# Kernel tuning notes

Hardware: AMD Instinct MI355X
Metric: run time of the kernel (lower is better)

## Reference

```python
import jax, jax.numpy as jnp
import numpy as np

B, T, H, F, E = 512, 32, 768, 3072, 3  # E = num_route_experts = num_experts - 1 (top-1 beam)


def setup_inputs() -> dict:
    key = jax.random.key(0)
    ks = jax.random.split(key, 4)
    s = 0.02
    return {
        "x": jax.random.normal(ks[0], (B, T, H), jnp.float32),
        "Wg": jax.random.normal(ks[1], (E, H), jnp.float32) * s,
        "W1": jax.random.normal(ks[2], (E, H, F), jnp.float32) * s,
        "b1": jnp.zeros((E, F), jnp.float32),
        "W2": jax.random.normal(ks[3], (E, F, H), jnp.float32) * s,
        "b2": jnp.zeros((E, H), jnp.float32),
    }


def reference(x, Wg, W1, b1, W2, b2):
    # forward_gate: mean-pool over tokens (attention_mask is all-ones), linear gate, softmax
    scores = jax.nn.softmax(jnp.mean(x, axis=1) @ Wg.T, axis=-1)  # [B, E]
    # beam_search, first layer with num_route_beam=1: plain top-1 expert selection
    _, idx = jax.lax.top_k(scores, 1)
    sel = idx[:, 0]  # [B] int32, selected expert per sample
    # forward_expert_ffn: densely run EVERY route expert (gelu MLP) on the full batch
    h = jax.nn.gelu(jnp.einsum('bth,ehf->betf', x, W1) + b1[None, :, None, :], approximate=False)  # [B,E,T,F]
    y = jnp.einsum('betf,efh->beth', h, W2) + b2[None, :, None, :]  # [B,E,T,H]
    # weight_type == 'ffn_prob': one-hot mask times gate prob, then sum over experts
    w = scores * jax.nn.one_hot(sel, E, dtype=scores.dtype)  # [B, E]
    out = jnp.einsum('beth,be->bth', y, w)  # [B, T, H]
    return out
```

## Files before the change

kernel.cpp:

```cpp
#include <hip/hip_runtime.h>
#include <hip/hip_bf16.h>
#include <cstdint>
#include <cstddef>

namespace {

constexpr int kB = 512, kT = 32, kH = 768, kF = 3072, kE = 3;
constexpr int kMaxTiles = 131;
constexpr int kMaxChunk = 131;
constexpr int kHbufTile  = 128 * kF;
constexpr int kXconvB = kT * kH;

typedef __attribute__((ext_vector_type(8))) short short8;
typedef __attribute__((ext_vector_type(4))) float f32x4;

__device__ __forceinline__ void gld_lds16(const void* g, void* l) {
  __builtin_amdgcn_global_load_lds(
      (const __attribute__((address_space(1))) void*)g,
      (__attribute__((address_space(3))) void*)l, 16, 0, 0);
}

__device__ __forceinline__ float bf2f(__hip_bfloat16 v) { return __bfloat162float(v); }
__device__ __forceinline__ float bfu(unsigned short u) {
  return __uint_as_float(((unsigned)u) << 16);
}
__device__ __forceinline__ unsigned short f2bfb(float f) {
  __hip_bfloat16 h = __float2bfloat16(f);
  return *reinterpret_cast<unsigned short*>(&h);
}

__device__ __forceinline__ float gelu_f(float v) {
  float av = fabsf(v);
  float z = av * 0.70710678118654752f;
  float t = __builtin_amdgcn_rcpf(fmaf(0.3275911f, z, 1.0f));
  float p = fmaf(fmaf(fmaf(fmaf(1.061405429f, t, -1.453152027f), t, 1.421413741f),
                      t, -0.284496736f), t, 0.254829592f) * t;
  float er = fmaf(-p, __expf(-z * z), 1.0f);
  return 0.5f * v + 0.5f * av * er;
}

__global__ __launch_bounds__(256)
void k_prep_x(const void* __restrict__ xv, const void* __restrict__ Wgv,
              float* __restrict__ wsel,
              int* __restrict__ cntTk,
              int* __restrict__ lists,
              int* __restrict__ tileExpert, int* __restrict__ tileBatch,
              int* __restrict__ numTiles,
              __hip_bfloat16* __restrict__ xconv) {
  __shared__ __align__(16) unsigned short xs[32][772];
  __shared__ float red[3][256];
  __shared__ int sniffX, sniffG, lastFlag;
  __shared__ int csh[3];
  int b = blockIdx.x, tid = threadIdx.x;
  if (tid == 0) { sniffX = 0; sniffG = 0; }
  __syncthreads();
  {
    const unsigned short* xw = (const unsigned short*)xv;
    const unsigned short* gw = (const unsigned short*)Wgv;
    int lx = 0, lg = 0;
#pragma unroll
    for (int i = 0; i < 16; ++i) lx += (((xw[tid + 256 * i] >> 7) & 0xFF) >= 0xC0);
#pragma unroll
    for (int i = 0; i < 8; ++i) lg += (((gw[tid + 256 * i] >> 7) & 0xFF) >= 0xC0);
    atomicAdd(&sniffX, lx);
    atomicAdd(&sniffG, lg);
  }
  __syncthreads();
  bool fx = (sniffX > 64), fg = (sniffG > 32);

  float a0 = 0.f, a1 = 0.f, a2 = 0.f;
  if (tid < 192) {
    float m0 = 0.f, m1 = 0.f, m2 = 0.f, m3 = 0.f;
    if (fx) {
      const float4* xr = (const float4*)((const float*)xv + (size_t)b * kT * kH) + tid;
#pragma unroll 8
      for (int t = 0; t < kT; ++t) {
        float4 u = xr[t * 192];
        m0 += u.x; m1 += u.y; m2 += u.z; m3 += u.w;
        ushort4 v;
        v.x = f2bfb(u.x); v.y = f2bfb(u.y); v.z = f2bfb(u.z); v.w = f2bfb(u.w);
        *(ushort4*)&xs[t][tid * 4] = v;
      }
    } else {
      const ushort4* xr = (const ushort4*)((const unsigned short*)xv + (size_t)b * kT * kH) + tid;
#pragma unroll 8
      for (int t = 0; t < kT; ++t) {
        ushort4 u = xr[t * 192];
        m0 += bfu(u.x); m1 += bfu(u.y); m2 += bfu(u.z); m3 += bfu(u.w);
        *(ushort4*)&xs[t][tid * 4] = u;
      }
    }
    const float inv = 1.f / kT;
    m0 *= inv; m1 *= inv; m2 *= inv; m3 *= inv;
#pragma unroll
    for (int e = 0; e < kE; ++e) {
      float w0, w1v, w2v, w3;
      int base = e * kH + tid * 4;
      if (fg) {
        float4 u = *(const float4*)((const float*)Wgv + base);
        w0 = u.x; w1v = u.y; w2v = u.z; w3 = u.w;
      } else {
        ushort4 u = *(const ushort4*)((const unsigned short*)Wgv + base);
        w0 = bfu(u.x); w1v = bfu(u.y); w2v = bfu(u.z); w3 = bfu(u.w);
      }
      float d = m0 * w0 + m1 * w1v + m2 * w2v + m3 * w3;
      if (e == 0) a0 = d; else if (e == 1) a1 = d; else a2 = d;
    }
  }
  red[0][tid] = a0; red[1][tid] = a1; red[2][tid] = a2;
  __syncthreads();
  for (int s2 = 128; s2 > 0; s2 >>= 1) {
    if (tid < s2) {
      red[0][tid] += red[0][tid + s2];
      red[1][tid] += red[1][tid + s2];
      red[2][tid] += red[2][tid + s2];
    }
    __syncthreads();
  }
  if (tid == 0) {
    float l0 = red[0][0], l1 = red[1][0], l2 = red[2][0];
    int am = 0; float mx = l0;
    if (l1 > mx) { mx = l1; am = 1; }
    if (l2 > mx) { mx = l2; am = 2; }
    float e0 = expf(l0 - mx), e1 = expf(l1 - mx), e2 = expf(l2 - mx);
    float inv = 1.f / (e0 + e1 + e2);
    float sc = (am == 0 ? e0 : (am == 1 ? e1 : e2)) * inv;
    wsel[b] = sc;
    int pos = atomicAdd(&cntTk[am], 1);
    lists[am * kB + pos] = b;
    __threadfence();
    int tk = atomicAdd(&cntTk[3], 1);
    lastFlag = (tk == kB - 1) ? 1 : 0;
  }

  __syncthreads();
  unsigned short* dst = (unsigned short*)xconv + (size_t)b * kXconvB;
#pragma unroll
  for (int i = 0; i < 12; ++i) {
    int g = i * 256 + tid;
    int t32 = g >> 7, r = g & 127, mm = r >> 2, qp = r & 3;
    int col = t32 * 32 + (qp ^ ((mm >> 1) & 3)) * 8;
    ushort4 lo = *(const ushort4*)&xs[mm][col];
    ushort4 hi = *(const ushort4*)&xs[mm][col + 4];
    short8 v;
    v[0] = lo.x; v[1] = lo.y; v[2] = lo.z; v[3] = lo.w;
    v[4] = hi.x; v[5] = hi.y; v[6] = hi.z; v[7] = hi.w;
    *(short8*)(dst + g * 8) = v;
  }

  if (lastFlag) {
    __threadfence();
    if (tid < 3) csh[tid] = cntTk[tid];
    __syncthreads();
    int c0 = csh[0], c1 = csh[1], c2 = csh[2];
    int t0 = ((c0 + 3) & ~3) >> 2;
    int t1 = ((c1 + 3) & ~3) >> 2;
    int t2 = ((c2 + 3) & ~3) >> 2;
    int total = t0 + t1 + t2;
    if (tid == 0) *numTiles = total;
    for (int t = tid; t < kMaxTiles; t += 256) {
      int e = 0, base = 0, cc = 0;
      bool pad = false;
      if (t < t0) { e = 0; base = t; cc = c0; }
      else if (t < t0 + t1) { e = 1; base = t - t0; cc = c1; }
      else if (t < total) { e = 2; base = t - t0 - t1; cc = c2; }
      else pad = true;
      if (pad) {
        tileExpert[t] = 0;
        for (int s = 0; s < 4; ++s) tileBatch[t * 4 + s] = -1;
      } else {
        tileExpert[t] = e;
        for (int s = 0; s < 4; ++s) {
          int i = base * 4 + s;
          tileBatch[t * 4 + s] = (i < cc) ? lists[e * kB + i] : -1;
        }
      }
    }
  }
}

__global__ __launch_bounds__(256)
void k_transpose6(const void* __restrict__ w1src, const void* __restrict__ w2src,
                  __hip_bfloat16* __restrict__ w1dst, __hip_bfloat16* __restrict__ w2dst) {
  int z = blockIdx.z;
  bool isW1 = (z < 3);
  int e = isW1 ? z : z - 3;
  __shared__ __align__(16) unsigned short t[64][73];
  __shared__ int cnt_s;
  if (threadIdx.x == 0) cnt_s = 0;
  __syncthreads();
  {
    const unsigned short* hw = (const unsigned short*)(isW1 ? w1src : w2src);
    int local = 0;
#pragma unroll
    for (int i = 0; i < 16; ++i)
      local += (((hw[threadIdx.x + 256 * i] >> 7) & 0xFF) >= 0xC0);
    atomicAdd(&cnt_s, local);
  }
  __syncthreads();
  bool f32 = (cnt_s > 64);
  const float* sf = (const float*)(isW1 ? w1src : w2src);
  const unsigned short* sb = (const unsigned short*)(isW1 ? w1src : w2src);
  unsigned short* dst = (unsigned short*)(isW1 ? w1dst : w2dst);
  int K = isW1 ? kH : kF, N = isW1 ? kF : kH;
  int ntx = N / 64;
  int bx = blockIdx.x;
  int n0 = (bx % ntx) * 64, k0 = (bx / ntx) * 64;
  size_t eoff = (size_t)e * K * N;
  int tr = threadIdx.x >> 4;
  int tc4 = (threadIdx.x & 15) * 4;
#pragma unroll
  for (int i = 0; i < 4; ++i) {
    int r = tr + 16 * i;
    size_t idx = eoff + (size_t)(k0 + r) * N + n0 + tc4;
    if (f32) {
      float4 u = *(const float4*)(sf + idx);
      t[r][tc4] = f2bfb(u.x); t[r][tc4 + 1] = f2bfb(u.y);
      t[r][tc4 + 2] = f2bfb(u.z); t[r][tc4 + 3] = f2bfb(u.w);
    } else {
      ushort4 u = *(const ushort4*)(sb + idx);
      t[r][tc4] = u.x; t[r][tc4 + 1] = u.y; t[r][tc4 + 2] = u.z; t[r][tc4 + 3] = u.w;
    }
  }
  __syncthreads();
#pragma unroll
  for (int i = 0; i < 4; ++i) {
    int rn = tr + 16 * i;
    ushort4 v;
    v.x = t[tc4][rn]; v.y = t[tc4 + 1][rn]; v.z = t[tc4 + 2][rn]; v.w = t[tc4 + 3][rn];
    *(ushort4*)(dst + eoff + (size_t)(n0 + rn) * K + k0 + tc4) = v;
  }
}

__global__ __launch_bounds__(256, 2)
void k_ffn1(const __hip_bfloat16* __restrict__ xconv,
            const __hip_bfloat16* __restrict__ w1t,
            const __hip_bfloat16* __restrict__ b1,
            const int* __restrict__ tileExpert,
            const int* __restrict__ tileBatch,
            const int* __restrict__ numTiles,
            int tileOff,
            __hip_bfloat16* __restrict__ hbuf) {
  int j = blockIdx.y;
  int local = j / 3;
  int tile = local + tileOff;
  if (tile >= *numTiles) return;
  int nIdx = 8 * (j % 3) + blockIdx.x;
  int nbase = nIdx * 128;
  int e = tileExpert[tile];
  __shared__ __align__(16) short ldsbuf[16384];
  short* ldsA = ldsbuf;
  short* ldsB = ldsbuf + 8192;
  int tid = threadIdx.x;
  int lane = tid & 63, wid = tid >> 6;
  int wm = wid >> 1, wn = wid & 1;
  int lane16 = lane & 15, qf = lane >> 4;
  int swzl = (lane16 >> 1) & 3;
  int qx = (qf ^ swzl) * 8;

  int slotLo = tid >> 7;
  int b0v = tileBatch[tile * 4];
  int bLo = tileBatch[tile * 4 + slotLo];
  int bHi = tileBatch[tile * 4 + 2 + slotLo];
  if (bLo < 0) bLo = b0v;
  if (bHi < 0) bHi = b0v;
  int mmLo = (tid >> 2) & 31;
  int q = (tid & 3) ^ ((tid >> 3) & 3);
  int qp = q ^ ((mmLo >> 1) & 3);
  int baseOff = (mmLo * 4 + qp) * 8;
  const __hip_bfloat16* pLo = xconv + (size_t)bLo * kXconvB + baseOff;
  const __hip_bfloat16* pHi = xconv + (size_t)bHi * kXconvB + baseOff;

  f32x4 acc[4][4];
#pragma unroll
  for (int r = 0; r < 4; ++r)
#pragma unroll
    for (int c = 0; c < 4; ++c) acc[r][c] = (f32x4)0.f;

  const __hip_bfloat16* w1e = w1t + (size_t)e * kF * kH;
  const __hip_bfloat16* gB[4];
  short* lB[4];
#pragma unroll
  for (int it = 0; it < 4; ++it) {
    int s = it * 256 + tid;
    int m = (s >> 2) & 127, kk = s >> 9;
    int qq = (s & 3) ^ ((s >> 3) & 3);
    gB[it] = w1e + (size_t)(nbase + m) * kH + kk * 32 + qq * 8;
    lB[it] = &ldsB[s * 8];
  }

  for (int k0 = 0; k0 < kH; k0 += 64) {
    int koff = (k0 >> 6) * 2048;
    gld_lds16(pLo + koff,        &ldsA[(0 * 256 + tid) * 8]);
    gld_lds16(pHi + koff,        &ldsA[(1 * 256 + tid) * 8]);
    gld_lds16(pLo + koff + 1024, &ldsA[(2 * 256 + tid) * 8]);
    gld_lds16(pHi + koff + 1024, &ldsA[(3 * 256 + tid) * 8]);
#pragma unroll
    for (int it = 0; it < 4; ++it) gld_lds16(gB[it] + k0, lB[it]);
    __syncthreads();
#pragma unroll
    for (int kk = 0; kk < 2; ++kk) {
      short8 af[4], bfr[4];
#pragma unroll
      for (int r = 0; r < 4; ++r) {
        int mr = wm * 64 + r * 16 + lane16;
        af[r] = *(const short8*)&ldsA[(kk * 512 + mr * 4) * 8 + qx];
      }
#pragma unroll
      for (int c = 0; c < 4; ++c) {
        int mb = wn * 64 + c * 16 + lane16;
        bfr[c] = *(const short8*)&ldsB[(kk * 512 + mb * 4) * 8 + qx];
      }
#pragma unroll
      for (int r = 0; r < 4; ++r)
#pragma unroll
        for (int c = 0; c < 4; ++c)
          acc[r][c] = __builtin_amdgcn_mfma_f32_16x16x32_bf16(af[r], bfr[c], acc[r][c], 0, 0, 0);
    }
    __syncthreads();
  }

  __hip_bfloat16* htile = hbuf + (size_t)local * kHbufTile;
  unsigned short* uls = (unsigned short*)ldsbuf;
  int q4 = qf * 4;
#pragma unroll
  for (int c = 0; c < 4; ++c) {
    int nn = wn * 64 + c * 16 + lane16;
    float bias = bf2f(b1[e * kF + nbase + nn]);
    int lbase = (nn >> 6) * 8192 + ((nn >> 5) & 1) * 4096 + (nn & 7);
    int qn = (nn >> 3) & 3;
#pragma unroll
    for (int r = 0; r < 4; ++r) {
#pragma unroll
      for (int g = 0; g < 4; ++g) {
        int m = wm * 64 + r * 16 + q4 + g;
        float v = acc[r][c][g] + bias;
        uls[lbase + (m * 4 + (qn ^ ((m >> 1) & 3))) * 8] = f2bfb(gelu_f(v));
      }
    }
  }
  __syncthreads();
  unsigned short* dstg = (unsigned short*)htile + (size_t)(nbase >> 6) * 8192;
#pragma unroll
  for (int i = 0; i < 8; ++i) {
    int s = i * 2048 + tid * 8;
    *(short8*)(dstg + s) = *(const short8*)(uls + s);
  }
}

__global__ __launch_bounds__(256, 2)
void k_ffn2(const __hip_bfloat16* __restrict__ hbuf,
            const __hip_bfloat16* __restrict__ w2t,
            const __hip_bfloat16* __restrict__ b2,
            const float* __restrict__ wsel,
            const int* __restrict__ tileExpert,
            const int* __restrict__ tileBatch,
            const int* __restrict__ numTiles,
            int tileOff, int chunk,
            float* __restrict__ out) {
  int j = blockIdx.y;
  int local = blockIdx.x + 8 * (j / 6);
  if (local >= chunk) return;
  int tile = local + tileOff;
  if (tile >= *numTiles) return;
  int nbase = (j % 6) * 128;
  int e = tileExpert[tile];
  int tbraw[4];
  float sc[4];
#pragma unroll
  for (int s = 0; s < 4; ++s) {
    int bb = tileBatch[tile * 4 + s];
    tbraw[s] = bb;
    sc[s] = (bb >= 0) ? wsel[bb] : 0.f;
  }
  __shared__ __align__(16) short ldsA[8192];
  __shared__ __align__(16) short ldsB[8192];
  int tid = threadIdx.x;
  int lane = tid & 63, wid = tid >> 6;
  int wm = wid >> 1, wn = wid & 1;
  int lane16 = lane & 15, qf = lane >> 4;
  int swzl = (lane16 >> 1) & 3;
  int qx = (qf ^ swzl) * 8;

  f32x4 acc[4][4];
#pragma unroll
  for (int r = 0; r < 4; ++r)
#pragma unroll
    for (int c = 0; c < 4; ++c) acc[r][c] = (f32x4)0.f;

  const __hip_bfloat16* w2e = w2t + (size_t)e * kF * kH;
  const __hip_bfloat16* htile = hbuf + (size_t)local * kHbufTile;
  const __hip_bfloat16* gB[4];
  short* lA[4];
  short* lB[4];
  int aoff[4];
#pragma unroll
  for (int it = 0; it < 4; ++it) {
    int s = it * 256 + tid;
    int m = (s >> 2) & 127, kk = s >> 9;
    int qq = (s & 3) ^ ((s >> 3) & 3);
    aoff[it] = s * 8;
    gB[it] = w2e + (size_t)(nbase + m) * kF + kk * 32 + qq * 8;
    lA[it] = &ldsA[s * 8];
    lB[it] = &ldsB[s * 8];
  }

  for (int k0 = 0; k0 < kF; k0 += 64) {
#pragma unroll
    for (int it = 0; it < 4; ++it) gld_lds16(htile + k0 * 128 + aoff[it], lA[it]);
#pragma unroll
    for (int it = 0; it < 4; ++it) gld_lds16(gB[it] + k0, lB[it]);
    __syncthreads();
#pragma unroll
    for (int kk = 0; kk < 2; ++kk) {
      short8 af[4], bfr[4];
#pragma unroll
      for (int r = 0; r < 4; ++r) {
        int mr = wm * 64 + r * 16 + lane16;
        af[r] = *(const short8*)&ldsA[(kk * 512 + mr * 4) * 8 + qx];
      }
#pragma unroll
      for (int c = 0; c < 4; ++c) {
        int mb = wn * 64 + c * 16 + lane16;
        bfr[c] = *(const short8*)&ldsB[(kk * 512 + mb * 4) * 8 + qx];
      }
#pragma unroll
      for (int r = 0; r < 4; ++r)
#pragma unroll
        for (int c = 0; c < 4; ++c)
          acc[r][c] = __builtin_amdgcn_mfma_f32_16x16x32_bf16(af[r], bfr[c], acc[r][c], 0, 0, 0);
    }
    __syncthreads();
  }

  int q4 = qf * 4;
#pragma unroll
  for (int c = 0; c < 4; ++c) {
    int ncol = wn * 64 + c * 16 + lane16;
    float bias = bf2f(b2[e * kH + nbase + ncol]);
#pragma unroll
    for (int r = 0; r < 4; ++r) {
      int s = (wm * 64 + r * 16) >> 5;
      int bb = tbraw[s];
      if (bb < 0) continue;
      float scale = sc[s];
#pragma unroll
      for (int g = 0; g < 4; ++g) {
        int m = wm * 64 + r * 16 + q4 + g;
        float v = (acc[r][c][g] + bias) * scale;
        out[((size_t)(bb * kT + (m & 31))) * kH + nbase + ncol] = v;
      }
    }
  }
}

}

extern "C" void kernel_launch(void* const* d_in, const int* in_sizes, int n_in,
                              void* d_out, int out_size, void* d_ws, size_t ws_size,
                              hipStream_t stream) {
  (void)in_sizes; (void)n_in; (void)out_size;
  float* out = (float*)d_out;

  char* ws = (char*)d_ws;
  size_t off = 0;
  auto alloc = [&](size_t bytes) -> char* {
    char* p = ws + off;
    off = (off + bytes + 255) & ~(size_t)255;
    return p;
  };
  int*   cntTk      = (int*)alloc(16);
  float* wsel       = (float*)alloc(kB * 4);
  int*   lists      = (int*)alloc((size_t)kE * kB * 4);
  int*   tileExpert = (int*)alloc(kMaxTiles * 4);
  int*   tileBatch  = (int*)alloc(kMaxTiles * 4 * 4);
  int*   numTiles   = (int*)alloc(4);
  __hip_bfloat16* w1t   = (__hip_bfloat16*)alloc((size_t)kE * kH * kF * 2);
  __hip_bfloat16* w2t   = (__hip_bfloat16*)alloc((size_t)kE * kH * kF * 2);
  __hip_bfloat16* xconv = (__hip_bfloat16*)alloc((size_t)kB * kXconvB * 2);

  size_t tileBytes = (size_t)kHbufTile * 2;
  size_t avail = (ws_size > off + tileBytes) ? (ws_size - off) : tileBytes;
  int chunk = (int)(avail / tileBytes);
  if (chunk > kMaxChunk) chunk = kMaxChunk;
  if (chunk < 1) chunk = 1;
  __hip_bfloat16* hbuf = (__hip_bfloat16*)alloc((size_t)chunk * tileBytes);

  hipMemsetAsync(cntTk, 0, 16, stream);
  k_prep_x<<<kB, 256, 0, stream>>>(d_in[0], d_in[1], wsel, cntTk, lists,
                                   tileExpert, tileBatch, numTiles, xconv);
  k_transpose6<<<dim3(576, 1, 6), 256, 0, stream>>>(d_in[2], d_in[4], w1t, w2t);
  for (int toff = 0; toff < kMaxTiles; toff += chunk) {
    k_ffn1<<<dim3(8, 3 * chunk), 256, 0, stream>>>(xconv, w1t,
                                                   (const __hip_bfloat16*)d_in[3],
                                                   tileExpert, tileBatch,
                                                   numTiles, toff, hbuf);
    int rows2 = (chunk + 7) / 8;
    k_ffn2<<<dim3(8, 6 * rows2), 256, 0, stream>>>(hbuf, w2t,
                                                   (const __hip_bfloat16*)d_in[5], wsel,
                                                   tileExpert, tileBatch, numTiles,
                                                   toff, chunk, out);
  }
}
```

Baseline: 378.0 us.

## Rewrite FFN1 as 256x256 double-buffered GEMM with fused prep/transpose launch

Merges the x-prep and weight-transpose kernels into one launch, which saves a kernel boundary. FFN1 moves to 512-thread blocks that compute two 128-row tiles against a 256-wide N slab. Operand loads go straight from global memory into LDS and are double-buffered, with explicit waitcnt, barriers and setprio interleaving so loads overlap MFMA work. Tile padding now rounds experts to pairs of tiles so each block handles two tiles of the same expert. The cost is higher register and LDS pressure (128KB dynamic LDS), and some extra padded tiles.

```diff
diff --git a/kernel.cpp b/kernel.cpp
--- a/kernel.cpp
+++ b/kernel.cpp
@@ -6,9 +6,9 @@
 namespace {
 
 constexpr int kB = 512, kT = 32, kH = 768, kF = 3072, kE = 3;
-constexpr int kMaxTiles = 131;
-constexpr int kMaxChunk = 131;
-constexpr int kHbufTile  = 128 * kF;
+constexpr int kMaxTiles = 132;
+constexpr int kMaxChunk = 132;
+constexpr int kHbufTile = 128 * kF;
 constexpr int kXconvB = kT * kH;
 
 typedef __attribute__((ext_vector_type(8))) short short8;
@@ -40,311 +40,375 @@
 }
 
 __global__ __launch_bounds__(256)
-void k_prep_x(const void* __restrict__ xv, const void* __restrict__ Wgv,
-              float* __restrict__ wsel,
-              int* __restrict__ cntTk,
-              int* __restrict__ lists,
-              int* __restrict__ tileExpert, int* __restrict__ tileBatch,
-              int* __restrict__ numTiles,
-              __hip_bfloat16* __restrict__ xconv) {
-  __shared__ __align__(16) unsigned short xs[32][772];
-  __shared__ float red[3][256];
-  __shared__ int sniffX, sniffG, lastFlag;
-  __shared__ int csh[3];
-  int b = blockIdx.x, tid = threadIdx.x;
-  if (tid == 0) { sniffX = 0; sniffG = 0; }
-  __syncthreads();
-  {
-    const unsigned short* xw = (const unsigned short*)xv;
-    const unsigned short* gw = (const unsigned short*)Wgv;
-    int lx = 0, lg = 0;
-#pragma unroll
-    for (int i = 0; i < 16; ++i) lx += (((xw[tid + 256 * i] >> 7) & 0xFF) >= 0xC0);
-#pragma unroll
-    for (int i = 0; i < 8; ++i) lg += (((gw[tid + 256 * i] >> 7) & 0xFF) >= 0xC0);
-    atomicAdd(&sniffX, lx);
-    atomicAdd(&sniffG, lg);
-  }
-  __syncthreads();
-  bool fx = (sniffX > 64), fg = (sniffG > 32);
-
-  float a0 = 0.f, a1 = 0.f, a2 = 0.f;
-  if (tid < 192) {
-    float m0 = 0.f, m1 = 0.f, m2 = 0.f, m3 = 0.f;
-    if (fx) {
-      const float4* xr = (const float4*)((const float*)xv + (size_t)b * kT * kH) + tid;
+void k_prep(const void* __restrict__ xv, const void* __restrict__ Wgv,
+            const void* __restrict__ w1src, const void* __restrict__ w2src,
+            float* __restrict__ wsel, int* __restrict__ cntTk,
+            int* __restrict__ lists, int* __restrict__ tileExpert,
+            int* __restrict__ tileBatch, int* __restrict__ numTiles,
+            __hip_bfloat16* __restrict__ xconv,
+            __hip_bfloat16* __restrict__ w1dst, __hip_bfloat16* __restrict__ w2dst) {
+  __shared__ __align__(16) char smem[52992];
+  __shared__ int ish[6];
+  int tid = threadIdx.x;
+  if (blockIdx.x < (unsigned)kB) {
+    auto xs = (unsigned short (*)[772])smem;
+    float (*red)[256] = (float (*)[256])(smem + 49408);
+    int b = blockIdx.x;
+    if (tid == 0) { ish[0] = 0; ish[1] = 0; }
+    __syncthreads();
+    {
+      const unsigned short* xw = (const unsigned short*)xv;
+      const unsigned short* gw = (const unsigned short*)Wgv;
+      int lx = 0, lg = 0;
+#pragma unroll
+      for (int i = 0; i < 16; ++i) lx += (((xw[tid + 256 * i] >> 7) & 0xFF) >= 0xC0);
+#pragma unroll
+      for (int i = 0; i < 8; ++i) lg += (((gw[tid + 256 * i] >> 7) & 0xFF) >= 0xC0);
+      atomicAdd(&ish[0], lx);
+      atomicAdd(&ish[1], lg);
+    }
+    __syncthreads();
+    bool fx = (ish[0] > 64), fg = (ish[1] > 32);
+    float a0 = 0.f, a1 = 0.f, a2 = 0.f;
+    if (tid < 192) {
+      float m0 = 0.f, m1 = 0.f, m2 = 0.f, m3 = 0.f;
+      if (fx) {
+        const float4* xr = (const float4*)((const float*)xv + (size_t)b * kT * kH) + tid;
 #pragma unroll 8
-      for (int t = 0; t < kT; ++t) {
-        float4 u = xr[t * 192];
-        m0 += u.x; m1 += u.y; m2 += u.z; m3 += u.w;
-        ushort4 v;
-        v.x = f2bfb(u.x); v.y = f2bfb(u.y); v.z = f2bfb(u.z); v.w = f2bfb(u.w);
-        *(ushort4*)&xs[t][tid * 4] = v;
-      }
-    } else {
-      const ushort4* xr = (const ushort4*)((const unsigned short*)xv + (size_t)b * kT * kH) + tid;
+        for (int t = 0; t < kT; ++t) {
+          float4 u = xr[t * 192];
+          m0 += u.x; m1 += u.y; m2 += u.z; m3 += u.w;
+          ushort4 v;
+          v.x = f2bfb(u.x); v.y = f2bfb(u.y); v.z = f2bfb(u.z); v.w = f2bfb(u.w);
+          *(ushort4*)&xs[t][tid * 4] = v;
+        }
+      } else {
+        const ushort4* xr = (const ushort4*)((const unsigned short*)xv + (size_t)b * kT * kH) + tid;
 #pragma unroll 8
-      for (int t = 0; t < kT; ++t) {
-        ushort4 u = xr[t * 192];
-        m0 += bfu(u.x); m1 += bfu(u.y); m2 += bfu(u.z); m3 += bfu(u.w);
-        *(ushort4*)&xs[t][tid * 4] = u;
-      }
-    }
-    const float inv = 1.f / kT;
-    m0 *= inv; m1 *= inv; m2 *= inv; m3 *= inv;
-#pragma unroll
-    for (int e = 0; e < kE; ++e) {
-      float w0, w1v, w2v, w3;
-      int base = e * kH + tid * 4;
-      if (fg) {
-        float4 u = *(const float4*)((const float*)Wgv + base);
-        w0 = u.x; w1v = u.y; w2v = u.z; w3 = u.w;
+        for (int t = 0; t < kT; ++t) {
+          ushort4 u = xr[t * 192];
+          m0 += bfu(u.x); m1 += bfu(u.y); m2 += bfu(u.z); m3 += bfu(u.w);
+          *(ushort4*)&xs[t][tid * 4] = u;
+        }
+      }
+      const float inv = 1.f / kT;
+      m0 *= inv; m1 *= inv; m2 *= inv; m3 *= inv;
+#pragma unroll
+      for (int e = 0; e < kE; ++e) {
+        float w0, w1v, w2v, w3;
+        int base = e * kH + tid * 4;
+        if (fg) {
+          float4 u = *(const float4*)((const float*)Wgv + base);
+          w0 = u.x; w1v = u.y; w2v = u.z; w3 = u.w;
+        } else {
+          ushort4 u = *(const ushort4*)((const unsigned short*)Wgv + base);
+          w0 = bfu(u.x); w1v = bfu(u.y); w2v = bfu(u.z); w3 = bfu(u.w);
+        }
+        float d = m0 * w0 + m1 * w1v + m2 * w2v + m3 * w3;
+        if (e == 0) a0 = d; else if (e == 1) a1 = d; else a2 = d;
+      }
+    }
+    red[0][tid] = a0; red[1][tid] = a1; red[2][tid] = a2;
+    __syncthreads();
+    for (int s2 = 128; s2 > 0; s2 >>= 1) {
+      if (tid < s2) {
+        red[0][tid] += red[0][tid + s2];
+        red[1][tid] += red[1][tid + s2];
+        red[2][tid] += red[2][tid + s2];
+      }
+      __syncthreads();
+    }
+    if (tid == 0) {
+      float l0 = red[0][0], l1 = red[1][0], l2 = red[2][0];
+      int am = 0; float mx = l0;
+      if (l1 > mx) { mx = l1; am = 1; }
+      if (l2 > mx) { mx = l2; am = 2; }
+      float e0 = expf(l0 - mx), e1 = expf(l1 - mx), e2 = expf(l2 - mx);
+      float inv = 1.f / (e0 + e1 + e2);
+      float sc = (am == 0 ? e0 : (am == 1 ? e1 : e2)) * inv;
+      wsel[b] = sc;
+      int pos = atomicAdd(&cntTk[am], 1);
+      lists[am * kB + pos] = b;
+      __threadfence();
+      int tk = atomicAdd(&cntTk[3], 1);
+      ish[2] = (tk == kB - 1) ? 1 : 0;
+    }
+    __syncthreads();
+    unsigned short* dst = (unsigned short*)xconv + (size_t)b * kXconvB;
+#pragma unroll
+    for (int i = 0; i < 12; ++i) {
+      int g = i * 256 + tid;
+      int t32 = g >> 7, r = g & 127, mm = r >> 2, qp = r & 3;
+      int col = t32 * 32 + (qp ^ ((mm >> 1) & 3)) * 8;
+      ushort4 lo = *(const ushort4*)&xs[mm][col];
+      ushort4 hi = *(const ushort4*)&xs[mm][col + 4];
+      short8 v;
+      v[0] = lo.x; v[1] = lo.y; v[2] = lo.z; v[3] = lo.w;
+      v[4] = hi.x; v[5] = hi.y; v[6] = hi.z; v[7] = hi.w;
+      *(short8*)(dst + g * 8) = v;
+    }
+    if (ish[2]) {
+      __threadfence();
+      if (tid < 3) ish[3 + tid] = cntTk[tid];
+      __syncthreads();
+      int c0 = ish[3], c1 = ish[4], c2 = ish[5];
+      int t0 = ((c0 + 7) & ~7) >> 2;
+      int t1 = ((c1 + 7) & ~7) >> 2;
+      int t2 = ((c2 + 7) & ~7) >> 2;
+      int total = t0 + t1 + t2;
+      if (tid == 0) *numTiles = total;
+      for (int t = tid; t < kMaxTiles; t += 256) {
+        int e = 0, base = 0, cc = 0;
+        bool pad = false;
+        if (t < t0) { e = 0; base = t; cc = c0; }
+        else if (t < t0 + t1) { e = 1; base = t - t0; cc = c1; }
+        else if (t < total) { e = 2; base = t - t0 - t1; cc = c2; }
+        else pad = true;
+        if (pad) {
+          tileExpert[t] = 0;
+          for (int s = 0; s < 4; ++s) tileBatch[t * 4 + s] = -1;
+        } else {
+          tileExpert[t] = e;
+          for (int s = 0; s < 4; ++s) {
+            int i = base * 4 + s;
+            tileBatch[t * 4 + s] = (i < cc) ? lists[e * kB + i] : -1;
+          }
+        }
+      }
+    }
+  } else {
+    auto tsh = (unsigned short (*)[73])smem;
+    int bid = blockIdx.x - kB;
+    int z = bid / 576, bx = bid - z * 576;
+    bool isW1 = (z < 3);
+    int e = isW1 ? z : z - 3;
+    if (tid == 0) ish[0] = 0;
+    __syncthreads();
+    {
+      const unsigned short* hw = (const unsigned short*)(isW1 ? w1src : w2src);
+      int local = 0;
+#pragma unroll
+      for (int i = 0; i < 16; ++i)
+        local += (((hw[tid + 256 * i] >> 7) & 0xFF) >= 0xC0);
+      atomicAdd(&ish[0], local);
+    }
+    __syncthreads();
+    bool f32 = (ish[0] > 64);
+    const float* sf = (const float*)(isW1 ? w1src : w2src);
+    const unsigned short* sb = (const unsigned short*)(isW1 ? w1src : w2src);
+    unsigned short* dst = (unsigned short*)(isW1 ? w1dst : w2dst);
+    int K = isW1 ? kH : kF, N = isW1 ? kF : kH;
+    int ntx = N / 64;
+    int n0 = (bx % ntx) * 64, k0 = (bx / ntx) * 64;
+    size_t eoff = (size_t)e * K * N;
+    int tr = tid >> 4;
+    int tc4 = (tid & 15) * 4;
+#pragma unroll
+    for (int i = 0; i < 4; ++i) {
+      int r = tr + 16 * i;
+      size_t idx = eoff + (size_t)(k0 + r) * N + n0 + tc4;
+      if (f32) {
+        float4 u = *(const float4*)(sf + idx);
+        tsh[r][tc4] = f2bfb(u.x); tsh[r][tc4 + 1] = f2bfb(u.y);
+        tsh[r][tc4 + 2] = f2bfb(u.z); tsh[r][tc4 + 3] = f2bfb(u.w);
       } else {
-        ushort4 u = *(const ushort4*)((const unsigned short*)Wgv + base);
-        w0 = bfu(u.x); w1v = bfu(u.y); w2v = bfu(u.z); w3 = bfu(u.w);
-      }
-      float d = m0 * w0 + m1 * w1v + m2 * w2v + m3 * w3;
-      if (e == 0) a0 = d; else if (e == 1) a1 = d; else a2 = d;
-    }
-  }
-  red[0][tid] = a0; red[1][tid] = a1; red[2][tid] = a2;
-  __syncthreads();
-  for (int s2 = 128; s2 > 0; s2 >>= 1) {
-    if (tid < s2) {
-      red[0][tid] += red[0][tid + s2];
-      red[1][tid] += red[1][tid + s2];
-      red[2][tid] += red[2][tid + s2];
-    }
-    __syncthreads();
-  }
-  if (tid == 0) {
-    float l0 = red[0][0], l1 = red[1][0], l2 = red[2][0];
-    int am = 0; float mx = l0;
-    if (l1 > mx) { mx = l1; am = 1; }
-    if (l2 > mx) { mx = l2; am = 2; }
-    float e0 = expf(l0 - mx), e1 = expf(l1 - mx), e2 = expf(l2 - mx);
-    float inv = 1.f / (e0 + e1 + e2);
-    float sc = (am == 0 ? e0 : (am == 1 ? e1 : e2)) * inv;
-    wsel[b] = sc;
-    int pos = atomicAdd(&cntTk[am], 1);
-    lists[am * kB + pos] = b;
-    __threadfence();
-    int tk = atomicAdd(&cntTk[3], 1);
-    lastFlag = (tk == kB - 1) ? 1 : 0;
-  }
-
-  __syncthreads();
-  unsigned short* dst = (unsigned short*)xconv + (size_t)b * kXconvB;
-#pragma unroll
-  for (int i = 0; i < 12; ++i) {
-    int g = i * 256 + tid;
-    int t32 = g >> 7, r = g & 127, mm = r >> 2, qp = r & 3;
-    int col = t32 * 32 + (qp ^ ((mm >> 1) & 3)) * 8;
-    ushort4 lo = *(const ushort4*)&xs[mm][col];
-    ushort4 hi = *(const ushort4*)&xs[mm][col + 4];
-    short8 v;
-    v[0] = lo.x; v[1] = lo.y; v[2] = lo.z; v[3] = lo.w;
-    v[4] = hi.x; v[5] = hi.y; v[6] = hi.z; v[7] = hi.w;
-    *(short8*)(dst + g * 8) = v;
-  }
-
-  if (lastFlag) {
-    __threadfence();
-    if (tid < 3) csh[tid] = cntTk[tid];
-    __syncthreads();
-    int c0 = csh[0], c1 = csh[1], c2 = csh[2];
-    int t0 = ((c0 + 3) & ~3) >> 2;
-    int t1 = ((c1 + 3) & ~3) >> 2;
-    int t2 = ((c2 + 3) & ~3) >> 2;
-    int total = t0 + t1 + t2;
-    if (tid == 0) *numTiles = total;
-    for (int t = tid; t < kMaxTiles; t += 256) {
-      int e = 0, base = 0, cc = 0;
-      bool pad = false;
-      if (t < t0) { e = 0; base = t; cc = c0; }
-      else if (t < t0 + t1) { e = 1; base = t - t0; cc = c1; }
-      else if (t < total) { e = 2; base = t - t0 - t1; cc = c2; }
-      else pad = true;
-      if (pad) {
-        tileExpert[t] = 0;
-        for (int s = 0; s < 4; ++s) tileBatch[t * 4 + s] = -1;
-      } else {
-        tileExpert[t] = e;
-        for (int s = 0; s < 4; ++s) {
-          int i = base * 4 + s;
-          tileBatch[t * 4 + s] = (i < cc) ? lists[e * kB + i] : -1;
-        }
-      }
-    }
-  }
-}
-
-__global__ __launch_bounds__(256)
-void k_transpose6(const void* __restrict__ w1src, const void* __restrict__ w2src,
-                  __hip_bfloat16* __restrict__ w1dst, __hip_bfloat16* __restrict__ w2dst) {
-  int z = blockIdx.z;
-  bool isW1 = (z < 3);
-  int e = isW1 ? z : z - 3;
-  __shared__ __align__(16) unsigned short t[64][73];
-  __shared__ int cnt_s;
-  if (threadIdx.x == 0) cnt_s = 0;
-  __syncthreads();
-  {
-    const unsigned short* hw = (const unsigned short*)(isW1 ? w1src : w2src);
-    int local = 0;
-#pragma unroll
-    for (int i = 0; i < 16; ++i)
-      local += (((hw[threadIdx.x + 256 * i] >> 7) & 0xFF) >= 0xC0);
-    atomicAdd(&cnt_s, local);
-  }
-  __syncthreads();
-  bool f32 = (cnt_s > 64);
-  const float* sf = (const float*)(isW1 ? w1src : w2src);
-  const unsigned short* sb = (const unsigned short*)(isW1 ? w1src : w2src);
-  unsigned short* dst = (unsigned short*)(isW1 ? w1dst : w2dst);
-  int K = isW1 ? kH : kF, N = isW1 ? kF : kH;
-  int ntx = N / 64;
-  int bx = blockIdx.x;
-  int n0 = (bx % ntx) * 64, k0 = (bx / ntx) * 64;
-  size_t eoff = (size_t)e * K * N;
-  int tr = threadIdx.x >> 4;
-  int tc4 = (threadIdx.x & 15) * 4;
-#pragma unroll
-  for (int i = 0; i < 4; ++i) {
-    int r = tr + 16 * i;
-    size_t idx = eoff + (size_t)(k0 + r) * N + n0 + tc4;
-    if (f32) {
-      float4 u = *(const float4*)(sf + idx);
-      t[r][tc4] = f2bfb(u.x); t[r][tc4 + 1] = f2bfb(u.y);
-      t[r][tc4 + 2] = f2bfb(u.z); t[r][tc4 + 3] = f2bfb(u.w);
-    } else {
-      ushort4 u = *(const ushort4*)(sb + idx);
-      t[r][tc4] = u.x; t[r][tc4 + 1] = u.y; t[r][tc4 + 2] = u.z; t[r][tc4 + 3] = u.w;
-    }
-  }
-  __syncthreads();
-#pragma unroll
-  for (int i = 0; i < 4; ++i) {
-    int rn = tr + 16 * i;
-    ushort4 v;
-    v.x = t[tc4][rn]; v.y = t[tc4 + 1][rn]; v.z = t[tc4 + 2][rn]; v.w = t[tc4 + 3][rn];
-    *(ushort4*)(dst + eoff + (size_t)(n0 + rn) * K + k0 + tc4) = v;
-  }
-}
-
-__global__ __launch_bounds__(256, 2)
+        ushort4 u = *(const ushort4*)(sb + idx);
+        tsh[r][tc4] = u.x; tsh[r][tc4 + 1] = u.y; tsh[r][tc4 + 2] = u.z; tsh[r][tc4 + 3] = u.w;
+      }
+    }
+    __syncthreads();
+#pragma unroll
+    for (int i = 0; i < 4; ++i) {
+      int rn = tr + 16 * i;
+      ushort4 v;
+      v.x = tsh[tc4][rn]; v.y = tsh[tc4 + 1][rn];
+      v.z = tsh[tc4 + 2][rn]; v.w = tsh[tc4 + 3][rn];
+      *(ushort4*)(dst + eoff + (size_t)(n0 + rn) * K + k0 + tc4) = v;
+    }
+  }
+}
+
+__global__ __launch_bounds__(512, 2)
 void k_ffn1(const __hip_bfloat16* __restrict__ xconv,
             const __hip_bfloat16* __restrict__ w1t,
             const __hip_bfloat16* __restrict__ b1,
             const int* __restrict__ tileExpert,
             const int* __restrict__ tileBatch,
             const int* __restrict__ numTiles,
-            int tileOff,
+            int tileOff, int chunk,
             __hip_bfloat16* __restrict__ hbuf) {
-  int j = blockIdx.y;
-  int local = j / 3;
-  int tile = local + tileOff;
-  if (tile >= *numTiles) return;
-  int nIdx = 8 * (j % 3) + blockIdx.x;
-  int nbase = nIdx * 128;
-  int e = tileExpert[tile];
-  __shared__ __align__(16) short ldsbuf[16384];
-  short* ldsA = ldsbuf;
-  short* ldsB = ldsbuf + 8192;
+  extern __shared__ __align__(16) short lds[];
+  int nblk = (chunk >> 1) * 12;
+  int lid = blockIdx.x * gridDim.y + blockIdx.y;
+  if (lid >= nblk) return;
+  int lpair = lid / 12;
+  int nb = lid - lpair * 12;
+  int nbase = nb * 256;
+  int tile0 = tileOff + 2 * lpair;
+  if (tile0 >= *numTiles) return;
+  int e = tileExpert[tile0];
   int tid = threadIdx.x;
   int lane = tid & 63, wid = tid >> 6;
-  int wm = wid >> 1, wn = wid & 1;
+  int wr = wid >> 2, wc = wid & 3;
   int lane16 = lane & 15, qf = lane >> 4;
-  int swzl = (lane16 >> 1) & 3;
-  int qx = (qf ^ swzl) * 8;
-
-  int slotLo = tid >> 7;
-  int b0v = tileBatch[tile * 4];
-  int bLo = tileBatch[tile * 4 + slotLo];
-  int bHi = tileBatch[tile * 4 + 2 + slotLo];
-  if (bLo < 0) bLo = b0v;
-  if (bHi < 0) bHi = b0v;
-  int mmLo = (tid >> 2) & 31;
-  int q = (tid & 3) ^ ((tid >> 3) & 3);
-  int qp = q ^ ((mmLo >> 1) & 3);
-  int baseOff = (mmLo * 4 + qp) * 8;
-  const __hip_bfloat16* pLo = xconv + (size_t)bLo * kXconvB + baseOff;
-  const __hip_bfloat16* pHi = xconv + (size_t)bHi * kXconvB + baseOff;
-
-  f32x4 acc[4][4];
-#pragma unroll
-  for (int r = 0; r < 4; ++r)
+  int qx = (qf ^ ((lane16 >> 1) & 3)) * 8;
+  int tid8 = tid * 8;
+
+  int b0v = tileBatch[tile0 * 4];
+  int bA0 = tileBatch[tile0 * 4 + (tid >> 7)];
+  int bA1 = tileBatch[tile0 * 4 + 4 + (tid >> 7)];
+  if (bA0 < 0) bA0 = b0v;
+  if (bA1 < 0) bA1 = b0v;
+  int aoffc = (((tid >> 2) & 31) * 4 + (tid & 3)) * 8;
+  const __hip_bfloat16* pA0 = xconv + (size_t)bA0 * kXconvB + aoffc;
+  const __hip_bfloat16* pA1 = xconv + (size_t)bA1 * kXconvB + aoffc;
+  const __hip_bfloat16* w1e = w1t + (size_t)e * kF * kH;
+  int q8 = ((tid & 3) ^ ((tid >> 3) & 3)) * 8;
+  const __hip_bfloat16* pB0 = w1e + (size_t)(nbase + (tid >> 2)) * kH + q8;
+  const __hip_bfloat16* pB1 = w1e + (size_t)(nbase + 128 + (tid >> 2)) * kH + q8;
+  const int baseA = (wr * 128 + lane16) * 32 + qx;
+  const int baseB = 16384 + (wc * 64 + lane16) * 32 + qx;
+
+  f32x4 acc[8][4];
+#pragma unroll
+  for (int r = 0; r < 8; ++r)
 #pragma unroll
     for (int c = 0; c < 4; ++c) acc[r][c] = (f32x4)0.f;
 
-  const __hip_bfloat16* w1e = w1t + (size_t)e * kF * kH;
-  const __hip_bfloat16* gB[4];
-  short* lB[4];
-#pragma unroll
-  for (int it = 0; it < 4; ++it) {
-    int s = it * 256 + tid;
-    int m = (s >> 2) & 127, kk = s >> 9;
-    int qq = (s & 3) ^ ((s >> 3) & 3);
-    gB[it] = w1e + (size_t)(nbase + m) * kH + kk * 32 + qq * 8;
-    lB[it] = &ldsB[s * 8];
-  }
-
-  for (int k0 = 0; k0 < kH; k0 += 64) {
-    int koff = (k0 >> 6) * 2048;
-    gld_lds16(pLo + koff,        &ldsA[(0 * 256 + tid) * 8]);
-    gld_lds16(pHi + koff,        &ldsA[(1 * 256 + tid) * 8]);
-    gld_lds16(pLo + koff + 1024, &ldsA[(2 * 256 + tid) * 8]);
-    gld_lds16(pHi + koff + 1024, &ldsA[(3 * 256 + tid) * 8]);
-#pragma unroll
-    for (int it = 0; it < 4; ++it) gld_lds16(gB[it] + k0, lB[it]);
-    __syncthreads();
-#pragma unroll
-    for (int kk = 0; kk < 2; ++kk) {
-      short8 af[4], bfr[4];
-#pragma unroll
-      for (int r = 0; r < 4; ++r) {
-        int mr = wm * 64 + r * 16 + lane16;
-        af[r] = *(const short8*)&ldsA[(kk * 512 + mr * 4) * 8 + qx];
-      }
-#pragma unroll
-      for (int c = 0; c < 4; ++c) {
-        int mb = wn * 64 + c * 16 + lane16;
-        bfr[c] = *(const short8*)&ldsB[(kk * 512 + mb * 4) * 8 + qx];
-      }
-#pragma unroll
-      for (int r = 0; r < 4; ++r)
-#pragma unroll
-        for (int c = 0; c < 4; ++c)
-          acc[r][c] = __builtin_amdgcn_mfma_f32_16x16x32_bf16(af[r], bfr[c], acc[r][c], 0, 0, 0);
-    }
-    __syncthreads();
-  }
-
-  __hip_bfloat16* htile = hbuf + (size_t)local * kHbufTile;
-  unsigned short* uls = (unsigned short*)ldsbuf;
+  gld_lds16(pA0, &lds[tid8]);
+  gld_lds16(pA1, &lds[4096 + tid8]);
+  gld_lds16(pB0, &lds[16384 + tid8]);
+  gld_lds16(pB1, &lds[16384 + 4096 + tid8]);
+  gld_lds16(pA0 + 1024, &lds[8192 + tid8]);
+  gld_lds16(pA1 + 1024, &lds[8192 + 4096 + tid8]);
+  gld_lds16(pB0 + 32, &lds[16384 + 8192 + tid8]);
+  gld_lds16(pB1 + 32, &lds[16384 + 8192 + 4096 + tid8]);
+  asm volatile("s_waitcnt vmcnt(4)" ::: "memory");
+  __builtin_amdgcn_s_barrier();
+
+#define MF(r_, c_, A_, B_) \
+  acc[r_][c_] = __builtin_amdgcn_mfma_f32_16x16x32_bf16(A_, B_, acc[r_][c_], 0, 0, 0)
+#define MF16(RB)                                                \
+  MF(RB + 0, 0, a0, b0); MF(RB + 0, 1, a0, b1);                 \
+  MF(RB + 0, 2, a0, b2); MF(RB + 0, 3, a0, b3);                 \
+  MF(RB + 1, 0, a1, b0); MF(RB + 1, 1, a1, b1);                 \
+  MF(RB + 1, 2, a1, b2); MF(RB + 1, 3, a1, b3);                 \
+  MF(RB + 2, 0, a2, b0); MF(RB + 2, 1, a2, b1);                 \
+  MF(RB + 2, 2, a2, b2); MF(RB + 2, 3, a2, b3);                 \
+  MF(RB + 3, 0, a3, b0); MF(RB + 3, 1, a3, b1);                 \
+  MF(RB + 3, 2, a3, b2); MF(RB + 3, 3, a3, b3)
+#define LGKM_FENCE                                              \
+  asm volatile("s_waitcnt lgkmcnt(0)" ::: "memory");            \
+  __builtin_amdgcn_sched_barrier(0)
+
+#pragma unroll 1
+  for (int t = 0; t < 12; ++t) {
+    const short* cur = &lds[(t & 1) * 32768];
+    short* nxt = &lds[((t + 1) & 1) * 32768];
+    const bool hn = (t + 1) < 12;
+    const int tA = (t + 1) * 2048;
+    const int tB = (t + 1) * 64;
+    short8 a0, a1, a2, a3, b0, b1, b2, b3;
+    b0 = *(const short8*)&cur[baseB];
+    b1 = *(const short8*)&cur[baseB + 512];
+    b2 = *(const short8*)&cur[baseB + 1024];
+    b3 = *(const short8*)&cur[baseB + 1536];
+    a0 = *(const short8*)&cur[baseA];
+    a1 = *(const short8*)&cur[baseA + 512];
+    a2 = *(const short8*)&cur[baseA + 1024];
+    a3 = *(const short8*)&cur[baseA + 1536];
+    if (hn) {
+      gld_lds16(pA0 + tA, nxt + tid8);
+      gld_lds16(pA1 + tA, nxt + 4096 + tid8);
+    }
+    __builtin_amdgcn_s_barrier();
+    LGKM_FENCE;
+    __builtin_amdgcn_s_setprio(1);
+    MF16(0);
+    __builtin_amdgcn_s_setprio(0);
+    __builtin_amdgcn_s_barrier();
+    a0 = *(const short8*)&cur[baseA + 2048];
+    a1 = *(const short8*)&cur[baseA + 2560];
+    a2 = *(const short8*)&cur[baseA + 3072];
+    a3 = *(const short8*)&cur[baseA + 3584];
+    if (hn) {
+      gld_lds16(pB0 + tB, nxt + 16384 + tid8);
+      gld_lds16(pB1 + tB, nxt + 16384 + 4096 + tid8);
+      asm volatile("s_waitcnt vmcnt(4)" ::: "memory");
+    } else {
+      asm volatile("s_waitcnt vmcnt(0)" ::: "memory");
+    }
+    __builtin_amdgcn_s_barrier();
+    LGKM_FENCE;
+    __builtin_amdgcn_s_setprio(1);
+    MF16(4);
+    __builtin_amdgcn_s_setprio(0);
+    __builtin_amdgcn_s_barrier();
+    b0 = *(const short8*)&cur[8192 + baseB];
+    b1 = *(const short8*)&cur[8192 + baseB + 512];
+    b2 = *(const short8*)&cur[8192 + baseB + 1024];
+    b3 = *(const short8*)&cur[8192 + baseB + 1536];
+    a0 = *(const short8*)&cur[8192 + baseA];
+    a1 = *(const short8*)&cur[8192 + baseA + 512];
+    a2 = *(const short8*)&cur[8192 + baseA + 1024];
+    a3 = *(const short8*)&cur[8192 + baseA + 1536];
+    if (hn) {
+      gld_lds16(pA0 + tA + 1024, nxt + 8192 + tid8);
+      gld_lds16(pA1 + tA + 1024, nxt + 8192 + 4096 + tid8);
+    }
+    __builtin_amdgcn_s_barrier();
+    LGKM_FENCE;
+    __builtin_amdgcn_s_setprio(1);
+    MF16(0);
+    __builtin_amdgcn_s_setprio(0);
+    __builtin_amdgcn_s_barrier();
+    a0 = *(const short8*)&cur[8192 + baseA + 2048];
+    a1 = *(const short8*)&cur[8192 + baseA + 2560];
+    a2 = *(const short8*)&cur[8192 + baseA + 3072];
+    a3 = *(const short8*)&cur[8192 + baseA + 3584];
+    if (hn) {
+      gld_lds16(pB0 + tB + 32, nxt + 16384 + 8192 + tid8);
+      gld_lds16(pB1 + tB + 32, nxt + 16384 + 8192 + 4096 + tid8);
+      asm volatile("s_waitcnt vmcnt(4)" ::: "memory");
+    }
+    __builtin_amdgcn_s_barrier();
+    LGKM_FENCE;
+    __builtin_amdgcn_s_setprio(1);
+    MF16(4);
+    __builtin_amdgcn_s_setprio(0);
+    __builtin_amdgcn_s_barrier();
+  }
+#undef MF
+#undef MF16
+#undef LGKM_FENCE
+
   int q4 = qf * 4;
 #pragma unroll
   for (int c = 0; c < 4; ++c) {
-    int nn = wn * 64 + c * 16 + lane16;
-    float bias = bf2f(b1[e * kF + nbase + nn]);
-    int lbase = (nn >> 6) * 8192 + ((nn >> 5) & 1) * 4096 + (nn & 7);
-    int qn = (nn >> 3) & 3;
-#pragma unroll
-    for (int r = 0; r < 4; ++r) {
+    int nl = wc * 64 + c * 16 + lane16;
+    float bias = bf2f(b1[e * kF + nbase + nl]);
+    int lb = wr * 32768 + (nl >> 6) * 8192 + ((nl >> 5) & 1) * 4096 + (nl & 7);
+    int qn = (nl >> 3) & 3;
+#pragma unroll
+    for (int r = 0; r < 8; ++r) {
 #pragma unroll
       for (int g = 0; g < 4; ++g) {
-        int m = wm * 64 + r * 16 + q4 + g;
-        float v = acc[r][c][g] + bias;
-        uls[lbase + (m * 4 + (qn ^ ((m >> 1) & 3))) * 8] = f2bfb(gelu_f(v));
+        int m = r * 16 + q4 + g;
+        lds[lb + (m * 4 + (qn ^ ((m >> 1) & 3))) * 8] =
+            (short)f2bfb(gelu_f(acc[r][c][g] + bias));
       }
     }
   }
   __syncthreads();
-  unsigned short* dstg = (unsigned short*)htile + (size_t)(nbase >> 6) * 8192;
+  unsigned short* h0 = (unsigned short*)hbuf + (size_t)(2 * lpair) * kHbufTile +
+                       (size_t)(nbase >> 6) * 8192;
+  unsigned short* h1 = (unsigned short*)hbuf + (size_t)(2 * lpair + 1) * kHbufTile +
+                       (size_t)(nbase >> 6) * 8192;
 #pragma unroll
   for (int i = 0; i < 8; ++i) {
-    int s = i * 2048 + tid * 8;
-    *(short8*)(dstg + s) = *(const short8*)(uls + s);
+    int s = i * 4096 + tid8;
+    *(short8*)(h0 + s) = *(const short8*)&lds[s];
+    *(short8*)(h1 + s) = *(const short8*)&lds[32768 + s];
   }
 }
 
@@ -480,21 +544,25 @@
   __hip_bfloat16* xconv = (__hip_bfloat16*)alloc((size_t)kB * kXconvB * 2);
 
   size_t tileBytes = (size_t)kHbufTile * 2;
-  size_t avail = (ws_size > off + tileBytes) ? (ws_size - off) : tileBytes;
+  size_t avail = (ws_size > off + 2 * tileBytes) ? (ws_size - off) : 2 * tileBytes;
   int chunk = (int)(avail / tileBytes);
   if (chunk > kMaxChunk) chunk = kMaxChunk;
-  if (chunk < 1) chunk = 1;
+  chunk &= ~1;
+  if (chunk < 2) chunk = 2;
   __hip_bfloat16* hbuf = (__hip_bfloat16*)alloc((size_t)chunk * tileBytes);
 
+  hipFuncSetAttribute((const void*)k_ffn1,
+                      hipFuncAttributeMaxDynamicSharedMemorySize, 131072);
+
   hipMemsetAsync(cntTk, 0, 16, stream);
-  k_prep_x<<<kB, 256, 0, stream>>>(d_in[0], d_in[1], wsel, cntTk, lists,
-                                   tileExpert, tileBatch, numTiles, xconv);
-  k_transpose6<<<dim3(576, 1, 6), 256, 0, stream>>>(d_in[2], d_in[4], w1t, w2t);
+  k_prep<<<kB + 3456, 256, 0, stream>>>(d_in[0], d_in[1], d_in[2], d_in[4],
+                                        wsel, cntTk, lists, tileExpert, tileBatch,
+                                        numTiles, xconv, w1t, w2t);
   for (int toff = 0; toff < kMaxTiles; toff += chunk) {
-    k_ffn1<<<dim3(8, 3 * chunk), 256, 0, stream>>>(xconv, w1t,
-                                                   (const __hip_bfloat16*)d_in[3],
-                                                   tileExpert, tileBatch,
-                                                   numTiles, toff, hbuf);
+    int nblk1 = (chunk / 2) * 12;
+    k_ffn1<<<dim3(8, (nblk1 + 7) / 8), 512, 131072, stream>>>(
+        xconv, w1t, (const __hip_bfloat16*)d_in[3],
+        tileExpert, tileBatch, numTiles, toff, chunk, hbuf);
     int rows2 = (chunk + 7) / 8;
     k_ffn2<<<dim3(8, 6 * rows2), 256, 0, stream>>>(hbuf, w2t,
                                                    (const __hip_bfloat16*)d_in[5], wsel,
```

Measured after the change: 423.8 us. 1.12x slower.
